# Performance work log

Hardware: AMD Instinct MI355X
Metric: run time of the kernel (lower is better)

## Reference

```python
import jax, jax.numpy as jnp
import numpy as np
import math

K_BRANCH = 8  # config['k']

def _selectors(n, k):
    # Static (trace-time) construction of per-level gather indices, mask=True branch.
    L = math.ceil(math.log(n) / math.log(k)) + 1
    rel = [0] + [math.ceil(n / k ** i) for i in range(L)]  # level sizes, leaves first
    Li = np.cumsum(np.array(rel))                          # level start offsets in node dim
    sels = []
    for l in range(L):
        m = rel[l + 1]
        i = np.arange(m)[:, None]
        anc = None
        if l < L - 1:
            m_next = rel[l + 2]
            j = np.arange(m_next)[None, :]
            cond = (j + 1) / m_next <= i / m
            anc = np.where(cond, Li[l + 1] + j, 0)
        s = np.arange(k)[None, :]
        ridx = np.minimum(i // k * k + s, m - 1)
        sib = np.where(ridx <= i, Li[l] + ridx, 0)  # rel/m <= i/m  <=>  rel <= i
        chi = None
        if l >= 1:
            m_prev = rel[l]
            c = np.arange(k)[None, :]
            ridx = np.minimum(i * k + c, m_prev - 1)
            cond = ridx / m_prev <= i / m
            chi = np.where(cond, Li[l - 1] + ridx, 0)
        sels.append((anc, sib, chi))
    return L, Li, sels

def _sdp(q, Kmat, Vmat, sel, d):
    keys = Kmat[:, :, sel, :]   # [b,h,m,w,d] gather
    vals = Vmat[:, :, sel, :]
    logits = jnp.einsum('bhnd,bhnkd->bhnk', q, keys) / math.sqrt(d)
    w = jax.nn.softmax(logits, axis=-1)
    return jnp.einsum('bhnk,bhnkd->bhnd', w, vals)

def setup_inputs() -> dict:
    key = jax.random.key(0)
    k1, k2, k3 = jax.random.split(key, 3)
    b, h, n_tot, d = 2, 4, 585, 128
    return {
        'Q': jax.random.normal(k1, (b, h, n_tot, d), dtype=jnp.float32),
        'K': jax.random.normal(k2, (b, h, n_tot, d), dtype=jnp.float32),
        'V': jax.random.normal(k3, (b, h, n_tot, d), dtype=jnp.float32),
        'n': 512,
    }

def reference(Q, K, V, n):
    k = K_BRANCH
    d = Q.shape[-1]
    L, Li, sels = _selectors(int(n), k)
    # Sequential bottom-up level updates: V at level l is rewritten before level l+1 reads it.
    for l in range(L):
        anc, sib, chi = sels[l]
        q = Q[:, :, Li[l]:Li[l + 1], :]
        out = _sdp(q, K, V, sib, d)
        if anc is not None:
            out = out + _sdp(q, K, V, anc, d)
        if chi is not None:
            out = out + _sdp(q, K, V, chi, d)
        V = V.at[:, :, Li[l]:Li[l + 1], :].set(out / 3.0)
    return V
```

## Files before the change

kernel.cpp:

```cpp
#include <hip/hip_runtime.h>
#include <math.h>

#define D 128
#define NTOT 585
#define SCALE 0.08838834764831845f
#define THIRD 0.33333333333333333f

__device__ __forceinline__ float rsum_c(float v) {
    v += __shfl_xor(v, 1, 64);
    v += __shfl_xor(v, 2, 64);
    v += __shfl_xor(v, 4, 64);
    return v;
}
__device__ __forceinline__ float rsum_s(float v) {
    v += __shfl_xor(v, 8, 64);
    v += __shfl_xor(v, 16, 64);
    v += __shfl_xor(v, 32, 64);
    return v;
}
__device__ __forceinline__ float rmax_s(float v) {
    v = fmaxf(v, __shfl_xor(v, 8, 64));
    v = fmaxf(v, __shfl_xor(v, 16, 64));
    v = fmaxf(v, __shfl_xor(v, 32, 64));
    return v;
}
__device__ __forceinline__ float dot16(const float4 q[4], const float* __restrict__ row, int c) {
    const float4* k = (const float4*)(row + (c << 4));
    float4 k0 = k[0], k1 = k[1], k2 = k[2], k3 = k[3];
    float p0 = q[0].x * k0.x + q[0].y * k0.y + q[0].z * k0.z + q[0].w * k0.w;
    float p1 = q[1].x * k1.x + q[1].y * k1.y + q[1].z * k1.z + q[1].w * k1.w;
    float p2 = q[2].x * k2.x + q[2].y * k2.y + q[2].z * k2.z + q[2].w * k2.w;
    float p3 = q[3].x * k3.x + q[3].y * k3.y + q[3].z * k3.z + q[3].w * k3.w;
    return (p0 + p1) + (p2 + p3);
}
__device__ __forceinline__ void vacc(float w, const float* __restrict__ row, int c, float4 acc[4]) {
    const float4* v = (const float4*)(row + (c << 4));
#pragma unroll
    for (int u = 0; u < 4; ++u) {
        float4 t = v[u];
        acc[u].x += w * t.x; acc[u].y += w * t.y; acc[u].z += w * t.z; acc[u].w += w * t.w;
    }
}
__device__ __forceinline__ void attend(const float4 q[4], const float* __restrict__ krow,
                                       const float* __restrict__ vrow, int c, float4 acc[4]) {
    float lg = rsum_c(dot16(q, krow, c)) * SCALE;
    float m = rmax_s(lg);
    float e = __expf(lg - m);
    float z = rsum_s(e);
    vacc(e / z, vrow, c, acc);
}
__device__ __forceinline__ void loadq(const float* __restrict__ qrow, int c, float4 q[4]) {
    const float4* qp = (const float4*)(qrow + (c << 4));
#pragma unroll
    for (int u = 0; u < 4; ++u) q[u] = qp[u];
}
__device__ __forceinline__ void butterfly_acc(float4 acc[4]) {
#pragma unroll
    for (int u = 0; u < 4; ++u) {
        acc[u].x = rsum_s(acc[u].x);
        acc[u].y = rsum_s(acc[u].y);
        acc[u].z = rsum_s(acc[u].z);
        acc[u].w = rsum_s(acc[u].w);
    }
}

__global__ __launch_bounds__(256) void level0_kernel(const float* __restrict__ Q,
                                                     const float* __restrict__ K,
                                                     const float* __restrict__ V,
                                                     float* __restrict__ Out) {
    const int gwave = (blockIdx.x * 256 + threadIdx.x) >> 6;
    const int lane = threadIdx.x & 63;
    const int s = lane >> 3, c = lane & 7;
    const int i = gwave & 511;
    const int bh = gwave >> 9;
    const float* Qb = Q + (size_t)bh * NTOT * D;
    const float* Kb = K + (size_t)bh * NTOT * D;
    const float* Vb = V + (size_t)bh * NTOT * D;
    float* Ob = Out + (size_t)bh * NTOT * D;

    float4 q4[4];
    loadq(Qb + (size_t)i * D, c, q4);
    float4 acc[4] = {{0,0,0,0},{0,0,0,0},{0,0,0,0},{0,0,0,0}};
    {
        const int r = (i & ~7) + s;
        const int idx = (r <= i) ? r : 0;
        attend(q4, Kb + (size_t)idx * D, Vb + (size_t)idx * D, c, acc);
    }
    {
        float lg[8];
        int idx[8];
#pragma unroll
        for (int r = 0; r < 8; ++r) {
            const int j = 8 * r + s;
            idx[r] = (8 * (j + 1) <= i) ? (512 + j) : 0;
            lg[r] = rsum_c(dot16(q4, Kb + (size_t)idx[r] * D, c)) * SCALE;
        }
        float m = lg[0];
#pragma unroll
        for (int r = 1; r < 8; ++r) m = fmaxf(m, lg[r]);
        m = rmax_s(m);
        float z = 0.f;
#pragma unroll
        for (int r = 0; r < 8; ++r) { lg[r] = __expf(lg[r] - m); z += lg[r]; }
        z = rsum_s(z);
        const float inv = 1.f / z;
#pragma unroll
        for (int r = 0; r < 8; ++r) vacc(lg[r] * inv, Vb + (size_t)idx[r] * D, c, acc);
    }
    butterfly_acc(acc);
    if (s == 0) {
        float4* orow = (float4*)(Ob + (size_t)i * D + (c << 4));
#pragma unroll
        for (int u = 0; u < 4; ++u)
            orow[u] = make_float4(acc[u].x * THIRD, acc[u].y * THIRD,
                                  acc[u].z * THIRD, acc[u].w * THIRD);
    }
}

__global__ __launch_bounds__(256) void level123_kernel(const float* __restrict__ Q,
                                                       const float* __restrict__ K,
                                                       const float* __restrict__ V,
                                                       float* __restrict__ Out) {
    const int gwave = (blockIdx.x * 256 + threadIdx.x) >> 6;
    const int lane = threadIdx.x & 63;
    const int s = lane >> 3, c = lane & 7;
    const int i = gwave & 63;
    const int bh = gwave >> 6;
    const float* Qb = Q + (size_t)bh * NTOT * D;
    const float* Kb = K + (size_t)bh * NTOT * D;
    const float* Vb = V + (size_t)bh * NTOT * D;
    float* Ob = Out + (size_t)bh * NTOT * D;

    float4 o1[4];
    {
        float4 q4[4];
        loadq(Qb + (size_t)(512 + i) * D, c, q4);
        float4 acc[4] = {{0,0,0,0},{0,0,0,0},{0,0,0,0},{0,0,0,0}};
        {
            const int r = (i & ~7) + s;
            const bool pass = (r <= i);
            const float* krow = Kb + (size_t)(pass ? 512 + r : 0) * D;
            const float* vrow = pass ? (Vb + (size_t)(512 + r) * D) : Ob;
            attend(q4, krow, vrow, c, acc);
        }
        {
            const bool pass = (8 * (s + 1) <= i);
            const float* krow = Kb + (size_t)(pass ? 576 + s : 0) * D;
            const float* vrow = pass ? (Vb + (size_t)(576 + s) * D) : Ob;
            attend(q4, krow, vrow, c, acc);
        }
        {
            const int idx = (s == 0) ? 8 * i : 0;
            attend(q4, Kb + (size_t)idx * D, Ob + (size_t)idx * D, c, acc);
        }
        butterfly_acc(acc);
#pragma unroll
        for (int u = 0; u < 4; ++u)
            o1[u] = make_float4(acc[u].x * THIRD, acc[u].y * THIRD,
                                acc[u].z * THIRD, acc[u].w * THIRD);
        if (s == 0) {
            float4* orow = (float4*)(Ob + (size_t)(512 + i) * D + (c << 4));
#pragma unroll
            for (int u = 0; u < 4; ++u) orow[u] = o1[u];
        }
    }

    if ((i & 7) == 0) {
        const int j = i >> 3;
        const float4* r0 = (const float4*)(Ob + (c << 4));
        float4 q2[4];
        loadq(Qb + (size_t)(576 + j) * D, c, q2);
        float4 acc[4] = {{0,0,0,0},{0,0,0,0},{0,0,0,0},{0,0,0,0}};
        {
            const bool pass = (s <= j);
            const float* krow = Kb + (size_t)(pass ? 576 + s : 0) * D;
            const float* vrow = pass ? (Vb + (size_t)(576 + s) * D) : Ob;
            attend(q2, krow, vrow, c, acc);
        }
        {
            const float* krow = (s == 0) ? (Kb + (size_t)(512 + 8 * j) * D) : Kb;
            float lg = rsum_c(dot16(q2, krow, c)) * SCALE;
            float m = rmax_s(lg);
            float e = __expf(lg - m);
            float z = rsum_s(e);
            const float w = e / z;
#pragma unroll
            for (int u = 0; u < 4; ++u) {
                float4 vv = (s == 0) ? o1[u] : r0[u];
                acc[u].x += w * vv.x; acc[u].y += w * vv.y;
                acc[u].z += w * vv.z; acc[u].w += w * vv.w;
            }
        }
        butterfly_acc(acc);
        float4 o2[4];
#pragma unroll
        for (int u = 0; u < 4; ++u) {
            float4 z = r0[u];
            o2[u] = make_float4((acc[u].x + z.x) * THIRD, (acc[u].y + z.y) * THIRD,
                                (acc[u].z + z.z) * THIRD, (acc[u].w + z.w) * THIRD);
        }
        if (s == 0) {
            float4* orow = (float4*)(Ob + (size_t)(576 + j) * D + (c << 4));
#pragma unroll
            for (int u = 0; u < 4; ++u) orow[u] = o2[u];
        }

        if (j == 0) {
            float4 q3[4];
            loadq(Qb + (size_t)584 * D, c, q3);
            const float* krow = (s == 0) ? (Kb + (size_t)576 * D) : Kb;
            float lg = rsum_c(dot16(q3, krow, c)) * SCALE;
            float m = rmax_s(lg);
            float e = __expf(lg - m);
            float z = rsum_s(e);
            const float w = e / z;
            float4 acc3[4];
#pragma unroll
            for (int u = 0; u < 4; ++u) {
                float4 vv = (s == 0) ? o2[u] : r0[u];
                acc3[u] = make_float4(w * vv.x, w * vv.y, w * vv.z, w * vv.w);
            }
            butterfly_acc(acc3);
            if (s == 0) {
                const float4* v584 = (const float4*)(Vb + (size_t)584 * D + (c << 4));
                float4* orow = (float4*)(Ob + (size_t)584 * D + (c << 4));
#pragma unroll
                for (int u = 0; u < 4; ++u) {
                    float4 bb = v584[u];
                    orow[u] = make_float4((acc3[u].x + bb.x) * THIRD,
                                          (acc3[u].y + bb.y) * THIRD,
                                          (acc3[u].z + bb.z) * THIRD,
                                          (acc3[u].w + bb.w) * THIRD);
                }
            }
        }
    }
}

extern "C" void kernel_launch(void* const* d_in, const int* in_sizes, int n_in,
                              void* d_out, int out_size, void* d_ws, size_t ws_size,
                              hipStream_t stream) {
    const float* Q = (const float*)d_in[0];
    const float* K = (const float*)d_in[1];
    const float* V = (const float*)d_in[2];
    float* Out = (float*)d_out;
    hipLaunchKernelGGL(level0_kernel, dim3(1024), dim3(256), 0, stream, Q, K, V, Out);
    hipLaunchKernelGGL(level123_kernel, dim3(128), dim3(256), 0, stream, Q, K, V, Out);
}
```

Measured before the change: 87.97 us.

## Fuse level kernels into one launch by recomputing needed level-0 rows

Merges the level-0 kernel and the upper-level kernel into a single launch. Waves past the first 4096 recompute the level-0 outputs they depend on (row 8i, plus row 0 written as a closed form 2/3·V[0]) in registers instead of reading them back from global memory. This removes the second launch and the serialization between the two kernels. The cost is some duplicated level-0 work in the upper-level waves and higher register use.

Result: no change. 87.80 us (-0.2%).

```diff
diff --git a/kernel.cpp b/kernel.cpp
--- a/kernel.cpp
+++ b/kernel.cpp
@@ -49,6 +49,19 @@
     float z = rsum_s(e);
     vacc(e / z, vrow, c, acc);
 }
+__device__ __forceinline__ void attend_reg(const float4 q[4], const float* __restrict__ krow,
+                                           const float4 vv[4], int c, float4 acc[4]) {
+    float lg = rsum_c(dot16(q, krow, c)) * SCALE;
+    float m = rmax_s(lg);
+    float e = __expf(lg - m);
+    float z = rsum_s(e);
+    const float w = e / z;
+#pragma unroll
+    for (int u = 0; u < 4; ++u) {
+        acc[u].x += w * vv[u].x; acc[u].y += w * vv[u].y;
+        acc[u].z += w * vv[u].z; acc[u].w += w * vv[u].w;
+    }
+}
 __device__ __forceinline__ void loadq(const float* __restrict__ qrow, int c, float4 q[4]) {
     const float4* qp = (const float4*)(qrow + (c << 4));
 #pragma unroll
@@ -64,23 +77,15 @@
     }
 }
 
-__global__ __launch_bounds__(256) void level0_kernel(const float* __restrict__ Q,
-                                                     const float* __restrict__ K,
-                                                     const float* __restrict__ V,
-                                                     float* __restrict__ Out) {
-    const int gwave = (blockIdx.x * 256 + threadIdx.x) >> 6;
-    const int lane = threadIdx.x & 63;
-    const int s = lane >> 3, c = lane & 7;
-    const int i = gwave & 511;
-    const int bh = gwave >> 9;
-    const float* Qb = Q + (size_t)bh * NTOT * D;
-    const float* Kb = K + (size_t)bh * NTOT * D;
-    const float* Vb = V + (size_t)bh * NTOT * D;
-    float* Ob = Out + (size_t)bh * NTOT * D;
-
+__device__ __forceinline__ void l0_compute(int i, int s, int c,
+                                           const float* __restrict__ Qb,
+                                           const float* __restrict__ Kb,
+                                           const float* __restrict__ Vb,
+                                           float4 acc[4]) {
     float4 q4[4];
     loadq(Qb + (size_t)i * D, c, q4);
-    float4 acc[4] = {{0,0,0,0},{0,0,0,0},{0,0,0,0},{0,0,0,0}};
+#pragma unroll
+    for (int u = 0; u < 4; ++u) acc[u] = make_float4(0.f, 0.f, 0.f, 0.f);
     {
         const int r = (i & ~7) + s;
         const int idx = (r <= i) ? r : 0;
@@ -108,28 +113,66 @@
         for (int r = 0; r < 8; ++r) vacc(lg[r] * inv, Vb + (size_t)idx[r] * D, c, acc);
     }
     butterfly_acc(acc);
-    if (s == 0) {
-        float4* orow = (float4*)(Ob + (size_t)i * D + (c << 4));
-#pragma unroll
-        for (int u = 0; u < 4; ++u)
-            orow[u] = make_float4(acc[u].x * THIRD, acc[u].y * THIRD,
-                                  acc[u].z * THIRD, acc[u].w * THIRD);
-    }
-}
-
-__global__ __launch_bounds__(256) void level123_kernel(const float* __restrict__ Q,
+}
+
+__global__ __launch_bounds__(256) void sequoia_onepass(const float* __restrict__ Q,
                                                        const float* __restrict__ K,
                                                        const float* __restrict__ V,
                                                        float* __restrict__ Out) {
     const int gwave = (blockIdx.x * 256 + threadIdx.x) >> 6;
     const int lane = threadIdx.x & 63;
     const int s = lane >> 3, c = lane & 7;
-    const int i = gwave & 63;
-    const int bh = gwave >> 6;
+
+    if (gwave < 4096) {
+        const int i = gwave & 511;
+        const int bh = gwave >> 9;
+        const float* Qb = Q + (size_t)bh * NTOT * D;
+        const float* Kb = K + (size_t)bh * NTOT * D;
+        const float* Vb = V + (size_t)bh * NTOT * D;
+        float* Ob = Out + (size_t)bh * NTOT * D;
+        float4 acc[4];
+        l0_compute(i, s, c, Qb, Kb, Vb, acc);
+        if (s == 0) {
+            float4* orow = (float4*)(Ob + (size_t)i * D + (c << 4));
+#pragma unroll
+            for (int u = 0; u < 4; ++u)
+                orow[u] = make_float4(acc[u].x * THIRD, acc[u].y * THIRD,
+                                      acc[u].z * THIRD, acc[u].w * THIRD);
+        }
+        return;
+    }
+
+    const int t = gwave - 4096;
+    const int i = t & 63;
+    const int bh = t >> 6;
     const float* Qb = Q + (size_t)bh * NTOT * D;
     const float* Kb = K + (size_t)bh * NTOT * D;
     const float* Vb = V + (size_t)bh * NTOT * D;
     float* Ob = Out + (size_t)bh * NTOT * D;
+
+    float4 v0n[4];
+    {
+        const float4* vp = (const float4*)(Vb + (c << 4));
+#pragma unroll
+        for (int u = 0; u < 4; ++u) {
+            float4 v = vp[u];
+            v0n[u] = make_float4(v.x * (2.f * THIRD), v.y * (2.f * THIRD),
+                                 v.z * (2.f * THIRD), v.w * (2.f * THIRD));
+        }
+    }
+
+    float4 o0[4];
+    if (i == 0) {
+#pragma unroll
+        for (int u = 0; u < 4; ++u) o0[u] = v0n[u];
+    } else {
+        float4 tmp[4];
+        l0_compute(8 * i, s, c, Qb, Kb, Vb, tmp);
+#pragma unroll
+        for (int u = 0; u < 4; ++u)
+            o0[u] = make_float4(tmp[u].x * THIRD, tmp[u].y * THIRD,
+                                tmp[u].z * THIRD, tmp[u].w * THIRD);
+    }
 
     float4 o1[4];
     {
@@ -140,18 +183,37 @@
             const int r = (i & ~7) + s;
             const bool pass = (r <= i);
             const float* krow = Kb + (size_t)(pass ? 512 + r : 0) * D;
-            const float* vrow = pass ? (Vb + (size_t)(512 + r) * D) : Ob;
-            attend(q4, krow, vrow, c, acc);
+            float4 vv[4];
+            if (pass) {
+                const float4* vp = (const float4*)(Vb + (size_t)(512 + r) * D + (c << 4));
+#pragma unroll
+                for (int u = 0; u < 4; ++u) vv[u] = vp[u];
+            } else {
+#pragma unroll
+                for (int u = 0; u < 4; ++u) vv[u] = v0n[u];
+            }
+            attend_reg(q4, krow, vv, c, acc);
         }
         {
             const bool pass = (8 * (s + 1) <= i);
             const float* krow = Kb + (size_t)(pass ? 576 + s : 0) * D;
-            const float* vrow = pass ? (Vb + (size_t)(576 + s) * D) : Ob;
-            attend(q4, krow, vrow, c, acc);
-        }
-        {
-            const int idx = (s == 0) ? 8 * i : 0;
-            attend(q4, Kb + (size_t)idx * D, Ob + (size_t)idx * D, c, acc);
+            float4 vv[4];
+            if (pass) {
+                const float4* vp = (const float4*)(Vb + (size_t)(576 + s) * D + (c << 4));
+#pragma unroll
+                for (int u = 0; u < 4; ++u) vv[u] = vp[u];
+            } else {
+#pragma unroll
+                for (int u = 0; u < 4; ++u) vv[u] = v0n[u];
+            }
+            attend_reg(q4, krow, vv, c, acc);
+        }
+        {
+            const float* krow = (s == 0) ? (Kb + (size_t)(8 * i) * D) : Kb;
+            float4 vv[4];
+#pragma unroll
+            for (int u = 0; u < 4; ++u) vv[u] = (s == 0) ? o0[u] : v0n[u];
+            attend_reg(q4, krow, vv, c, acc);
         }
         butterfly_acc(acc);
 #pragma unroll
@@ -167,38 +229,36 @@
 
     if ((i & 7) == 0) {
         const int j = i >> 3;
-        const float4* r0 = (const float4*)(Ob + (c << 4));
         float4 q2[4];
         loadq(Qb + (size_t)(576 + j) * D, c, q2);
         float4 acc[4] = {{0,0,0,0},{0,0,0,0},{0,0,0,0},{0,0,0,0}};
         {
             const bool pass = (s <= j);
             const float* krow = Kb + (size_t)(pass ? 576 + s : 0) * D;
-            const float* vrow = pass ? (Vb + (size_t)(576 + s) * D) : Ob;
-            attend(q2, krow, vrow, c, acc);
+            float4 vv[4];
+            if (pass) {
+                const float4* vp = (const float4*)(Vb + (size_t)(576 + s) * D + (c << 4));
+#pragma unroll
+                for (int u = 0; u < 4; ++u) vv[u] = vp[u];
+            } else {
+#pragma unroll
+                for (int u = 0; u < 4; ++u) vv[u] = v0n[u];
+            }
+            attend_reg(q2, krow, vv, c, acc);
         }
         {
             const float* krow = (s == 0) ? (Kb + (size_t)(512 + 8 * j) * D) : Kb;
-            float lg = rsum_c(dot16(q2, krow, c)) * SCALE;
-            float m = rmax_s(lg);
-            float e = __expf(lg - m);
-            float z = rsum_s(e);
-            const float w = e / z;
-#pragma unroll
-            for (int u = 0; u < 4; ++u) {
-                float4 vv = (s == 0) ? o1[u] : r0[u];
-                acc[u].x += w * vv.x; acc[u].y += w * vv.y;
-                acc[u].z += w * vv.z; acc[u].w += w * vv.w;
-            }
+            float4 vv[4];
+#pragma unroll
+            for (int u = 0; u < 4; ++u) vv[u] = (s == 0) ? o1[u] : v0n[u];
+            attend_reg(q2, krow, vv, c, acc);
         }
         butterfly_acc(acc);
         float4 o2[4];
 #pragma unroll
-        for (int u = 0; u < 4; ++u) {
-            float4 z = r0[u];
-            o2[u] = make_float4((acc[u].x + z.x) * THIRD, (acc[u].y + z.y) * THIRD,
-                                (acc[u].z + z.z) * THIRD, (acc[u].w + z.w) * THIRD);
-        }
+        for (int u = 0; u < 4; ++u)
+            o2[u] = make_float4((acc[u].x + v0n[u].x) * THIRD, (acc[u].y + v0n[u].y) * THIRD,
+                                (acc[u].z + v0n[u].z) * THIRD, (acc[u].w + v0n[u].w) * THIRD);
         if (s == 0) {
             float4* orow = (float4*)(Ob + (size_t)(576 + j) * D + (c << 4));
 #pragma unroll
@@ -217,7 +277,7 @@
             float4 acc3[4];
 #pragma unroll
             for (int u = 0; u < 4; ++u) {
-                float4 vv = (s == 0) ? o2[u] : r0[u];
+                float4 vv = (s == 0) ? o2[u] : v0n[u];
                 acc3[u] = make_float4(w * vv.x, w * vv.y, w * vv.z, w * vv.w);
             }
             butterfly_acc(acc3);
@@ -244,6 +304,5 @@
     const float* K = (const float*)d_in[1];
     const float* V = (const float*)d_in[2];
     float* Out = (float*)d_out;
-    hipLaunchKernelGGL(level0_kernel, dim3(1024), dim3(256), 0, stream, Q, K, V, Out);
-    hipLaunchKernelGGL(level123_kernel, dim3(128), dim3(256), 0, stream, Q, K, V, Out);
-}
+    hipLaunchKernelGGL(sequoia_onepass, dim3(1152), dim3(256), 0, stream, Q, K, V, Out);
+}
```
